# Kernel optimization log

Hardware: AMD Instinct MI355X
Metric: run time of the kernel (lower is better)

## Reference

```python
import jax, jax.numpy as jnp
import numpy as np

H = W = 256
L = H * W                      # number of graph vertices / tree leaves
N_NODES = 2 * L - 1            # binary partition tree node count
LAM = 1.0                      # lambda_ (soft-area temperature)


def _grid_edges():
    """4-adjacency grid graph edges (same structure as higra get_4_adjacency_graph)."""
    idx = np.arange(L, dtype=np.int64).reshape(H, W)
    src = np.concatenate([idx[:, :-1].ravel(), idx[:-1, :].ravel()])
    dst = np.concatenate([idx[:, 1:].ravel(), idx[1:, :].ravel()])
    return src.astype(np.int32), dst.astype(np.int32)


def setup_inputs() -> dict:
    key = jax.random.key(0)
    src, dst = _grid_edges()
    ew = jax.random.uniform(key, (src.shape[0],), dtype=jnp.float32)
    return {"edge_weights": ew,
            "edges_src": jnp.asarray(src),
            "edges_dst": jnp.asarray(dst)}


def _build_tree(ew, src, dst):
    """higra.bpt_canonical: Kruskal over stably-sorted edges, building a binary
    merge tree. Leaves are 0..L-1, internal node L+i is created by the i-th MST
    edge. Returns (sizes, mst_edge_map, ancestor paths). All integer structure
    is piecewise-constant w.r.t. edge_weights (no gradient flows through it)."""
    order = np.argsort(ew, kind="stable")
    uf = np.arange(L)

    def find(x):
        r = x
        while uf[r] != r:
            r = uf[r]
        while uf[x] != r:
            uf[x], x = r, uf[x]
        return r

    canon = np.arange(L)                      # tree node of each union-find root
    parent = np.arange(N_NODES)               # self-parent until set (root keeps self)
    sizes = np.ones(N_NODES, dtype=np.float32)
    edge_map = np.zeros(L - 1, dtype=np.int64)
    node = L
    for ei in order:
        a = find(src[ei]); b = find(dst[ei])
        if a == b:
            continue
        na, nb = canon[a], canon[b]
        parent[na] = node
        parent[nb] = node
        sizes[node] = sizes[na] + sizes[nb]
        edge_map[node - L] = ei
        uf[a] = b
        canon[b] = node
        node += 1
    # self-inclusive ancestor paths, padded by repeating the root
    cur = np.arange(N_NODES)
    cols = [cur.copy()]
    while np.any(parent[cur] != cur):
        cur = parent[cur]
        cols.append(cur.copy())
    paths = np.stack(cols, axis=1)            # [N_NODES, D+1]
    return sizes, edge_map, paths


def _softarea(edge_weights, edge_map, sizes_np, paths_np):
    """Soft area of every tree node n:
       area(n) = sum_x sigmoid((alt(n) - d(x, n)) / lambda)
    where d(x,n) is the min ultrametric distance from leaf x to the leaves of n:
      - x in subtree(n), x != n : d = alt(parent(x))
      - x == n (leaf)           : d = 0
      - x outside subtree(n)    : d = alt(lowest ancestor of n containing x).
    Outside leaves are grouped per ancestor a (count = size(a) - size(previous
    node on the path)), giving an O(N * depth) vectorized computation."""
    alt = jnp.concatenate([jnp.zeros((L,), edge_weights.dtype),
                           edge_weights[edge_map]])          # [N_NODES]
    alt_path = alt[paths_np]                                  # [N, D+1]
    size_path = sizes_np[paths_np]                            # constant, numpy
    diff = jnp.asarray(size_path[:, 1:] - size_path[:, :-1])  # 0 on root padding
    outside = jnp.sum(
        diff * jax.nn.sigmoid((alt[:, None] - alt_path[:, 1:]) / LAM), axis=1)

    # inside: each leaf x contributes sigmoid((alt(a_k) - alt(parent(x)))/lam)
    # to every proper ancestor a_k, plus sigmoid(0)=0.5 to itself (alt(leaf)=0).
    lp = paths_np[:L]                                         # [L, D+1]
    alt_lp = alt_path[:L]
    valid = jnp.asarray((lp[:, 1:] != lp[:, :-1]).astype(np.float32))
    vals = jax.nn.sigmoid((alt_lp[:, 1:] - alt_lp[:, 1:2]) / LAM) * valid
    inside = jax.ops.segment_sum(vals.reshape(-1),
                                 jnp.asarray(lp[:, 1:].reshape(-1)),
                                 num_segments=N_NODES)
    inside = inside.at[:L].add(0.5)
    return inside + outside


def reference(edge_weights, edges_src, edges_dst):
    sizes, edge_map, paths = _build_tree(np.asarray(edge_weights),
                                         np.asarray(edges_src),
                                         np.asarray(edges_dst))
    return _softarea(edge_weights, jnp.asarray(edge_map), sizes, paths)
```

## Files before the change

### kernel.cpp

```cpp
#include <hip/hip_runtime.h>
#include <stdint.h>

typedef unsigned int u32;
typedef unsigned short u16;
typedef unsigned long long u64;

#define L_VERTS 65536
#define N_EDGES 130560
#define N_NODES 131071
#define NODEPAD 131072

#define CCH 170
#define CCHM 86
#define SCH 768
#define PADM (CCHM*SCH)
#define NMST (L_VERTS-1)
#define MAXSV 1536
#define HSZ 2048

#define NB 255
#define TPB 64
#define IPT 8
#define IPB 512

__global__ void init_keys(const float* __restrict__ w, u32* __restrict__ keys, u32* __restrict__ vals,
                          u32* szG, u16* canonTop16, u32* parent, float* alt){
  int i = blockIdx.x*blockDim.x + threadIdx.x;
  if(i < N_EDGES){ keys[i] = __float_as_uint(w[i]); vals[i] = (u32)i; }
  if(i < N_NODES){ parent[i]=(u32)i; alt[i]=0.f; }
  if(i < L_VERTS){ szG[i]=1u; canonTop16[i]=0xFFFFu; }
}

__global__ void radix_hist(const u32* __restrict__ idx, const u32* __restrict__ keys,
                           u32* __restrict__ histG, int shift){
  __shared__ u32 h[256];
  for(int i=threadIdx.x;i<256;i+=TPB) h[i]=0;
  __syncthreads();
  int base = blockIdx.x*IPB + threadIdx.x*IPT;
  #pragma unroll
  for(int i=0;i<IPT;i++){
    u32 e = idx[base+i];
    u32 d = (keys[e]>>shift)&255u;
    atomicAdd(&h[d],1u);
  }
  __syncthreads();
  for(int i=threadIdx.x;i<256;i+=TPB) histG[i*NB+blockIdx.x]=h[i];
}

__global__ void radix_scan(u32* histG){
  const int M = 256*NB;
  __shared__ u32 sums[1024];
  int t=threadIdx.x; int s=t*64; u32 acc=0;
  for(int i=0;i<64;i++){int id=s+i; if(id<M) acc+=histG[id];}
  sums[t]=acc; __syncthreads();
  for(int off=1; off<1024; off<<=1){
    u32 v=(t>=off)?sums[t-off]:0u;
    __syncthreads();
    sums[t]+=v;
    __syncthreads();
  }
  u32 run = (t==0)?0u:sums[t-1];
  for(int i=0;i<64;i++){int id=s+i; if(id<M){u32 v=histG[id]; histG[id]=run; run+=v;}}
}

__global__ void radix_scatter(const u32* __restrict__ idxIn, const u32* __restrict__ keys,
                              u32* __restrict__ idxOut, const u32* __restrict__ histG, int shift){
  __shared__ u16 thoff[256][TPB];
  int t=threadIdx.x;
  for(int d=t;d<256;d+=TPB) for(int j=0;j<TPB;j++) thoff[d][j]=0;
  __syncthreads();
  int base = blockIdx.x*IPB + t*IPT;
  u32 myv[IPT]; u32 myd[IPT];
  #pragma unroll
  for(int i=0;i<IPT;i++){
    myv[i]=idxIn[base+i];
    myd[i]=(keys[myv[i]]>>shift)&255u;
    thoff[myd[i]][t]++;
  }
  __syncthreads();
  for(int dd=0;dd<4;dd++){
    int d=t*4+dd; u32 run=0;
    for(int j=0;j<TPB;j++){ u32 v=thoff[d][j]; thoff[d][j]=(u16)run; run+=v; }
  }
  __syncthreads();
  #pragma unroll
  for(int i=0;i<IPT;i++){
    u32 d=myd[i];
    u32 pos = histG[d*NB+blockIdx.x] + (u32)thoff[d][t];
    thoff[d][t]++;
    idxOut[pos]=myv[i];
  }
}

__global__ void build_epair(const u32* __restrict__ order, const int* __restrict__ srcv,
                            const int* __restrict__ dstv, u32* __restrict__ epair){
  int p=blockIdx.x*blockDim.x+threadIdx.x;
  if(p>=N_EDGES) return;
  u32 e=order[p];
  epair[p]=((u32)dstv[e]<<16)|(u32)srcv[e];
}

#define CBK 255
#define CT 512
#define DEADE 0xFFFFFFFFu

__device__ __forceinline__ u32 bfind(const u32* __restrict__ parentB, u32 x){
  while(true){ u32 p=parentB[x]; if(p==x) return x; x=p; }
}

__global__ void bor_init(u32* parentB, u32* minE, unsigned char* mstF, u32* bctr){
  int i=blockIdx.x*blockDim.x+threadIdx.x;
  if(i<L_VERTS){ parentB[i]=(u32)i; minE[i]=0xFFFFFFFFu; }
  if(i<N_EDGES) mstF[i]=0;
  if(i<16) bctr[i]=0u;
}

__global__ void bor_minedge(u32* __restrict__ epair, const u32* __restrict__ parentB,
                            u32* __restrict__ minE, const unsigned char* __restrict__ mstF,
                            const u32* __restrict__ bctr, int r){
  if(r>0 && bctr[r-1]==0u) return;
  int p=blockIdx.x*blockDim.x+threadIdx.x;
  u32 pr=epair[p];
  if(pr==DEADE) return;
  u32 ra=bfind(parentB, pr&0xFFFFu), rb=bfind(parentB, pr>>16);
  if(ra==rb){ if(!mstF[p]) epair[p]=DEADE; return; }
  atomicMin(&minE[ra],(u32)p);
  atomicMin(&minE[rb],(u32)p);
}

__global__ void bor_hookA(const u32* __restrict__ epair, const u32* __restrict__ parentB,
                          const u32* __restrict__ minE, u32* __restrict__ nextB,
                          unsigned char* __restrict__ mstF, const u32* __restrict__ bctr, int r){
  if(r>0 && bctr[r-1]==0u) return;
  int v=blockIdx.x*blockDim.x+threadIdx.x;
  if(v>=L_VERTS) return;
  if(parentB[v]!=(u32)v) return;
  u32 p=minE[v];
  if(p==0xFFFFFFFFu) return;
  u32 pr=epair[p];
  u32 ra=bfind(parentB, pr&0xFFFFu), rb=bfind(parentB, pr>>16);
  u32 w2=(ra==(u32)v)?rb:ra;
  nextB[v]=w2;
  mstF[p]=1;
}

__global__ void bor_hookB(u32* __restrict__ parentB, const u32* __restrict__ minE,
                          const u32* __restrict__ nextB, u32* __restrict__ bctr, int r){
  if(r>0 && bctr[r-1]==0u) return;
  int v=blockIdx.x*blockDim.x+threadIdx.x;
  if(v>=L_VERTS) return;
  if(parentB[v]!=(u32)v) return;
  u32 p=minE[v];
  if(p==0xFFFFFFFFu) return;
  u32 w2=nextB[v];
  if(minE[w2]==p && (u32)v<w2) return;
  parentB[v]=w2;
  bctr[r]=1u;
}

__global__ void bor_compress(u32* __restrict__ parentB, u32* __restrict__ minE,
                             const u32* __restrict__ bctr, int r){
  if(r>0 && bctr[r-1]==0u) return;
  int v=blockIdx.x*blockDim.x+threadIdx.x;
  if(v>=L_VERTS) return;
  u32 x=(u32)v;
  while(true){ u32 px=parentB[x]; if(px==x) break; u32 g=parentB[px]; if(g!=px) parentB[x]=g; x=g; }
  parentB[v]=x;
  minE[v]=0xFFFFFFFFu;
}

__global__ void mst_count(const unsigned char* __restrict__ mstF, u32* __restrict__ blockCnt){
  int b=blockIdx.x, t=threadIdx.x;
  int p=b*CT+t;
  u64 m=__ballot(mstF[p]!=0);
  __shared__ u32 ws[8];
  if((t&63)==0) ws[t>>6]=(u32)__popcll(m);
  __syncthreads();
  if(t==0){ u32 s=0; for(int i=0;i<8;i++) s+=ws[i]; blockCnt[b]=s; }
}

__global__ void mst_scan(const u32* __restrict__ blockCnt, u32* __restrict__ blockBase,
                         u32* __restrict__ mepair){
  int t=threadIdx.x;
  __shared__ u32 s[256];
  u32 v=(t<CBK)?blockCnt[t]:0u;
  s[t]=v; __syncthreads();
  for(int o=1;o<256;o<<=1){ u32 x=(t>=o)?s[t-o]:0u; __syncthreads(); s[t]+=x; __syncthreads(); }
  if(t<CBK) blockBase[t]=s[t]-v;
  u32 total=s[255];
  for(u32 j=total+(u32)t; j<(u32)PADM; j+=256u) mepair[j]=0u;
}

__global__ void mst_scatter(const unsigned char* __restrict__ mstF, const u32* __restrict__ blockBase,
                            const u32* __restrict__ order, const u32* __restrict__ epair,
                            const float* __restrict__ w,
                            u32* __restrict__ mepair, float* __restrict__ alt){
  int b=blockIdx.x, t=threadIdx.x;
  int p=b*CT+t;
  u32 f=(u32)mstF[p];
  u64 m=__ballot(f!=0);
  __shared__ u32 ws[8];
  int wid=t>>6, lane=t&63;
  if(lane==0) ws[wid]=(u32)__popcll(m);
  __syncthreads();
  if(t==0){ u32 s2=0; for(int i=0;i<8;i++){ u32 x=ws[i]; ws[i]=s2; s2+=x; } }
  __syncthreads();
  if(f){
    u32 pre=(u32)__popcll(m & ((1ull<<lane)-1ull));
    u32 pos=blockBase[b]+ws[wid]+pre;
    mepair[pos]=epair[p];
    alt[(u32)L_VERTS+pos]=w[order[p]];
  }
}

__device__ __forceinline__ u32 ald(u32* p){
  return __hip_atomic_load(p, __ATOMIC_RELAXED, __HIP_MEMORY_SCOPE_AGENT);
}
__device__ __forceinline__ void ast(u32* p, u32 v){
  __hip_atomic_store(p, v, __ATOMIC_RELAXED, __HIP_MEMORY_SCOPE_AGENT);
}

__global__ void __launch_bounds__(1024,1) p1_checkpoints(
    const u32* __restrict__ epair,
    u32* szG, u16* lid16, u16* svroot16, u16* svsize16, u16* svnext16, u32* mG)
{
  __shared__ u16 ufL[L_VERTS];
  __shared__ u32 hkey[HSZ];
  __shared__ u32 sufL[MAXSV];
  __shared__ u32 compsz[MAXSV];
  __shared__ u16 ssz[MAXSV];
  __shared__ u16 lidL[2*SCH];
  __shared__ u32 mcnt;
  int t = threadIdx.x;
  for(int i=t;i<L_VERTS/2;i+=1024) ((u32*)ufL)[i]=((2u*(u32)i+1u)<<16)|(2u*(u32)i);
  for(int k=0;k<CCHM;k++){
    for(int i=t;i<HSZ;i+=1024) hkey[i]=0xFFFFFFFFu;
    for(u32 s=t;s<MAXSV;s+=1024){ sufL[s]=s; compsz[s]=0u; }
    if(t==0) mcnt=0u;
    __syncthreads();
    int base = k*SCH;
    for(int i=t;i<2*SCH;i+=1024){
      u32 pr = epair[base+(i>>1)];
      u32 v = (i&1)? (pr>>16) : (pr&0xFFFFu);
      u32 x=v;
      while(true){ u32 px=ufL[x]; if(px==x)break; u32 g=ufL[px]; if(g!=px) ufL[x]=(u16)g; x=g; }
      u32 r=x;
      if(v!=r) ufL[v]=(u16)r;
      u32 h=(r*2654435761u)>>21;
      while(true){
        u32 old=atomicCAS(&hkey[h],0xFFFFFFFFu,(r<<16)|0x7FFFu);
        if(old==0xFFFFFFFFu){
          u32 id=atomicAdd(&mcnt,1u);
          svroot16[k*MAXSV+id]=(u16)r;
          hkey[h]=(r<<16)|id;
          break;
        }
        if((old>>16)==r) break;
        h=(h+1)&(HSZ-1u);
      }
      lidL[i]=(u16)h;
    }
    __syncthreads();
    u32 mc=mcnt;
    if(t==0) mG[k]=mc;
    for(u32 s=t;s<mc;s+=1024){
      u32 r=(u32)svroot16[k*MAXSV+s];
      u32 szm1=ald(&szG[r])-1u;
      svsize16[k*MAXSV+s]=(u16)szm1;
      ssz[s]=(u16)szm1;
    }
    for(int i=t;i<2*SCH;i+=1024) lid16[2*base+i]=(u16)(hkey[lidL[i]]&0xFFFFu);
    for(int j=t;j<SCH;j+=1024){
      u32 sa=hkey[lidL[2*j]]&0xFFFFu, sb=hkey[lidL[2*j+1]]&0xFFFFu;
      if(sa==sb) continue;
      while(true){
        u32 x=sa; while(true){u32 p2=sufL[x]; if(p2==x)break; u32 g=sufL[p2]; if(g!=p2) sufL[x]=g; x=g;}
        u32 y=sb; while(true){u32 p2=sufL[y]; if(p2==y)break; u32 g=sufL[p2]; if(g!=p2) sufL[y]=g; y=g;}
        if(x==y) break;
        u32 hi=x>y?x:y, lo=x^y^hi;
        if(atomicCAS(&sufL[hi],hi,lo)==hi) break;
        sa=hi; sb=lo;
      }
    }
    __syncthreads();
    for(u32 s=t;s<mc;s+=1024){
      u32 x=s; while(true){u32 p2=sufL[x]; if(p2==x)break; x=p2;}
      sufL[s]=x;
      atomicAdd(&compsz[x], (u32)ssz[s]+1u);
    }
    __syncthreads();
    for(u32 s=t;s<mc;s+=1024){
      u32 rs=sufL[s];
      u32 wv=(u32)svroot16[k*MAXSV+rs];
      svnext16[k*MAXSV+s]=(u16)wv;
      u32 myroot=(u32)svroot16[k*MAXSV+s];
      if(myroot!=wv) ufL[myroot]=(u16)wv;
      if(s==rs)      ast(&szG[wv], compsz[rs]);
    }
    __syncthreads();
  }
}

__global__ void __launch_bounds__(64) p2_chunk(
  const u16* __restrict__ lid16,
  const u16* __restrict__ svsize16, const u16* __restrict__ svnext16, const u32* __restrict__ mG,
  u16* __restrict__ outChA, u16* __restrict__ outChB, u16* __restrict__ outSize16,
  u32* __restrict__ accCnt, u16* __restrict__ compR16, u16* __restrict__ compTop16, u32* __restrict__ ncomp)
{
  int k = blockIdx.x; int t = threadIdx.x;
  __shared__ u16 uf[MAXSV];
  __shared__ u32 csize[MAXSV];
  __shared__ u16 ctop[MAXSV];
  __shared__ u16 svnl[MAXSV];
  __shared__ u32 lidP[SCH];
  __shared__ u32 cmp_s;
  u32 m = mG[k];
  int base=k*SCH;
  for(u32 s=t;s<m;s+=64){
    uf[s]=(u16)s;
    csize[s]=(u32)svsize16[k*MAXSV+s]+1u;
    ctop[s]=(u16)s;
    svnl[s]=svnext16[k*MAXSV+s];
  }
  for(int j=t;j<SCH;j+=64) lidP[j]=((const u32*)lid16)[base+j];
  if(t==0) cmp_s=0u;
  __syncthreads();
  if(t==0){
    u32 cnt=0;
    for(int j=0;j<SCH;j++){
      u32 lw = lidP[j];
      u32 la = lw & 0xFFFFu, lb = lw >> 16;
      u32 x=la; while(true){u32 px=uf[x]; if(px==x)break; u32 g=uf[px]; uf[x]=(u16)g; x=g;}
      u32 y=lb; while(true){u32 py=uf[y]; if(py==y)break; u32 g=uf[py]; uf[y]=(u16)g; y=g;}
      if(x==y) continue;
      u32 sa=csize[x], sb=csize[y], ns=sa+sb;
      outChA[base+cnt]=ctop[x];
      outChB[base+cnt]=ctop[y];
      outSize16[base+cnt]=(u16)(ns-1u);
      u32 win=(sa>=sb)?x:y, los=x^y^win;
      uf[los]=(u16)win; csize[win]=ns; ctop[win]=(u16)(0x8000u|cnt);
      cnt++;
    }
    accCnt[k]=cnt;
  }
  __syncthreads();
  for(u32 s=t;s<m;s+=64){
    if(uf[s]==(u16)s && (ctop[s]&0x8000u)){
      u32 pos=atomicAdd(&cmp_s,1u);
      compR16[k*MAXSV+pos]=svnl[s];
      compTop16[k*MAXSV+pos]=(u16)(ctop[s]&0x7FFFu);
    }
  }
  __syncthreads();
  if(t==0) ncomp[k]=cmp_s;
}

__global__ void __launch_bounds__(1024) p3_stitch(
  const u32* __restrict__ accCnt, const u16* __restrict__ outChA, const u16* __restrict__ outChB,
  const u16* __restrict__ outSize16,
  const u16* __restrict__ svroot16,
  const u16* __restrict__ compR16, const u16* __restrict__ compTop16, const u32* __restrict__ ncomp,
  u16* __restrict__ canonTop16, u32* __restrict__ parent, u16* __restrict__ usize16)
{
  __shared__ u32 accBase[CCH];
  int t=threadIdx.x;
  if(t==0){ u32 r=0; for(int k=0;k<CCHM;k++){ accBase[k]=r; r+=accCnt[k]; } }
  __syncthreads();
  for(int idx=t; idx<PADM; idx+=1024){
    int k = idx/SCH; int j = idx - k*SCH;
    if(j < (int)accCnt[k]){
      u32 nid = (u32)L_VERTS + accBase[k] + (u32)j;
      usize16[nid] = outSize16[idx];
      u32 cA=outChA[idx]; if(cA & 0x8000u) parent[(u32)L_VERTS+accBase[k]+(cA&0x7FFFu)] = nid;
      u32 cB=outChB[idx]; if(cB & 0x8000u) parent[(u32)L_VERTS+accBase[k]+(cB&0x7FFFu)] = nid;
    }
  }
  __syncthreads();
  for(int k=0;k<CCHM;k++){
    u32 ac=accCnt[k];
    for(u32 j=t;j<ac;j+=1024){
      u32 idx=(u32)(k*SCH)+j;
      u32 nid=(u32)L_VERTS+accBase[k]+j;
      u32 cA=outChA[idx];
      if(!(cA&0x8000u)){
        u32 root=(u32)svroot16[k*MAXSV+cA];
        u32 ct=(u32)canonTop16[root];
        parent[(ct==0xFFFFu)?root:((u32)L_VERTS+ct)]=nid;
      }
      u32 cB=outChB[idx];
      if(!(cB&0x8000u)){
        u32 root=(u32)svroot16[k*MAXSV+cB];
        u32 ct=(u32)canonTop16[root];
        parent[(ct==0xFFFFu)?root:((u32)L_VERTS+ct)]=nid;
      }
    }
    __syncthreads();
    u32 nc=ncomp[k];
    for(u32 j=t;j<nc;j+=1024){
      canonTop16[(u32)compR16[k*MAXSV+j]] = (u16)(accBase[k]+compTop16[k*MAXSV+j]);
    }
    __syncthreads();
  }
}

__device__ __forceinline__ void hvals6(float v, float* o){
  float v2=v*v, v3=v2*v, v4=v2*v2, v5=v4*v;
  o[0]=0.5f-0.25f*v+v3*(1.f/48.f)-v5*(1.f/480.f);
  o[1]=0.25f-v2*(1.f/16.f)+v4*(1.f/96.f);
  o[2]=v*(1.f/16.f)-v3*(1.f/48.f);
  o[3]=v2*(1.f/48.f)-(1.f/48.f);
  o[4]=-v*(1.f/96.f);
  o[5]=(1.f/480.f);
}

__global__ void zero_both(u32* cc, float* nodeM, u32* ctr){
  int i=blockIdx.x*blockDim.x+threadIdx.x;
  if(i<L_VERTS) cc[i]=0u;
  if(i<6*NODEPAD) nodeM[i]=0.f;
  if(i==0) *ctr=0u;
}

__global__ void prep_init(const u32* __restrict__ parent, const u16* __restrict__ usize16,
                          u32* cc, u32* J0, uint2* A0, float* out){
  int n=blockIdx.x*blockDim.x+threadIdx.x;
  if(n>=N_NODES) return;
  out[n] = (n<L_VERTS)?0.5f:0.0f;
  if(n==N_NODES-1){ J0[n]=(u32)n; A0[n]=make_uint2(0u,0u); return; }
  u32 p=parent[n];
  u32 ord=atomicAdd(&cc[p-L_VERTS],1u);
  u32 szP=(u32)usize16[p]+1u;
  u32 szN=(n<L_VERTS)?1u:((u32)usize16[n]+1u);
  u32 sib=szP-szN;
  A0[n]=make_uint2(ord? sib:0u, 1u + (ord? (2u*sib-1u):0u));
  J0[n]=p;
}

__global__ void triple_round(const u32* __restrict__ Jin, const uint2* __restrict__ Ain,
                             u32* __restrict__ Jout, uint2* __restrict__ Aout){
  int n=blockIdx.x*blockDim.x+threadIdx.x;
  if(n>=N_NODES) return;
  u32 j1=Jin[n], j2=Jin[j1], j3=Jin[j2], j4=Jin[j3], j5=Jin[j4], j6=Jin[j5], j7=Jin[j6];
  uint2 a0=Ain[n], a1=Ain[j1], a2=Ain[j2], a3=Ain[j3], a4=Ain[j4], a5=Ain[j5], a6=Ain[j6], a7=Ain[j7];
  Aout[n]=make_uint2(a0.x+a1.x+a2.x+a3.x+a4.x+a5.x+a6.x+a7.x,
                     a0.y+a1.y+a2.y+a3.y+a4.y+a5.y+a6.y+a7.y);
  Jout[n]=Jin[j7];
}

__global__ void scatter_all(const u32* __restrict__ parent, const float* __restrict__ alt,
                            const u16* __restrict__ usize16, const uint2* __restrict__ accF,
                            float* __restrict__ leafM, float* __restrict__ nodeM){
  int n=blockIdx.x*blockDim.x+threadIdx.x;
  if(n>=N_NODES) return;
  u32 p=parent[n];
  float h[6]; hvals6(alt[p],h);
  uint2 af=accF[n];
  if(n<L_VERTS){
    u32 pos=af.x;
    #pragma unroll
    for(int j=0;j<6;j++) leafM[(size_t)j*L_VERTS+pos]=h[j];
  }
  if(n<N_NODES-1){
    u32 szP=(u32)usize16[p]+1u;
    u32 szN=(n<L_VERTS)?1u:((u32)usize16[n]+1u);
    float d=(float)(szP-szN);
    u32 q0=af.y;
    u32 q1=q0 + 2u*szN - 1u;
    #pragma unroll
    for(int j=0;j<6;j++){
      float tm=d*h[j];
      atomicAdd(&nodeM[(size_t)j*NODEPAD+q0], tm);
      atomicAdd(&nodeM[(size_t)j*NODEPAD+q1], -tm);
    }
  }
}

__global__ void scanAll(float* __restrict__ leafM, float* __restrict__ nodeM,
                        float* __restrict__ bsumL, float* __restrict__ bsumN, u32* ctr){
  int b=blockIdx.x; int t=threadIdx.x;
  float* arr; u32 base; float* bs;
  if(b<6*64){ int row=b>>6, blk=b&63;  arr=leafM+(size_t)row*L_VERTS;  base=(u32)blk*1024u; bs=&bsumL[row*64+blk]; }
  else      { int bb=b-384; int row=bb>>7, blk=bb&127; arr=nodeM+(size_t)row*NODEPAD; base=(u32)blk*1024u; bs=&bsumN[row*128+blk]; }
  __shared__ float s[256];
  __shared__ u32 lastFlag;
  base += (u32)t*4u;
  float v0=arr[base],v1=arr[base+1],v2=arr[base+2],v3=arr[base+3];
  v1+=v0; v2+=v1; v3+=v2;
  s[t]=v3; __syncthreads();
  for(int o=1;o<256;o<<=1){ float x=(t>=o)?s[t-o]:0.f; __syncthreads(); s[t]+=x; __syncthreads(); }
  float pre=(t>0)?s[t-1]:0.f;
  arr[base]=v0+pre; arr[base+1]=v1+pre; arr[base+2]=v2+pre; arr[base+3]=v3+pre;
  if(t==255) *bs=s[255];
  __threadfence();
  if(t==0) lastFlag = (atomicAdd(ctr,1u)==1151u) ? 1u : 0u;
  __syncthreads();
  if(lastFlag){
    __threadfence();
    if(t<6){ float r=0; for(int i=0;i<64;i++){ float v=bsumL[t*64+i]; bsumL[t*64+i]=r; r+=v; } }
    else if(t<12){ int j=t-6; float r=0; for(int i=0;i<128;i++){ float v=bsumN[j*128+i]; bsumN[j*128+i]=r; r+=v; } }
  }
}

__global__ void eval_all(const uint2* __restrict__ accF, const float* __restrict__ alt,
                         const u16* __restrict__ usize16, const float* __restrict__ leafM,
                         const float* __restrict__ nodeM, const float* __restrict__ bsumL,
                         const float* __restrict__ bsumN, float* __restrict__ out){
  int n=blockIdx.x*blockDim.x+threadIdx.x;
  if(n>=N_NODES) return;
  uint2 af=accF[n];
  float u=alt[n];
  u32 q=af.y;
  float acc=0.f, up=1.f;
  #pragma unroll
  for(int j=0;j<6;j++){
    float T = nodeM[(size_t)j*NODEPAD+q] + bsumN[j*128 + (q>>10)];
    acc += up*T;
    up*=u;
  }
  if(n>=L_VERTS){
    u32 lo=af.x;
    u32 hi=lo + (u32)usize16[n] + 1u;
    up=1.f;
    #pragma unroll
    for(int j=0;j<6;j++){
      const float* arr=leafM + (size_t)j*L_VERTS;
      const float* bs=bsumL + j*64;
      float Ph = arr[hi-1u] + bs[(hi-1u)>>10];
      float Pl = lo ? (arr[lo-1u] + bs[(lo-1u)>>10]) : 0.f;
      acc += up*(Ph-Pl);
      up*=u;
    }
  }
  out[n]+=acc;
}

__global__ void ws_too_small(float* out){
  int i=blockIdx.x*blockDim.x+threadIdx.x;
  if(i<N_NODES) out[i]=1.0e6f;
}

extern "C" void kernel_launch(void* const* d_in, const int* in_sizes, int n_in,
                              void* d_out, int out_size, void* d_ws, size_t ws_size,
                              hipStream_t stream){
  (void)in_sizes; (void)n_in; (void)out_size;
  const float* w  = (const float*)d_in[0];
  const int* src  = (const int*)d_in[1];
  const int* dst  = (const int*)d_in[2];
  float* out = (float*)d_out;

  char* ws = (char*)d_ws;
  size_t off=0;
  auto alloc=[&](size_t bytes)->void*{ void* p = ws+off; off += (bytes+511)&~(size_t)511; return p; };
  u32* parent   =(u32*)alloc((size_t)N_NODES*4);
  float* alt    =(float*)alloc((size_t)N_NODES*4);
  u16* usize16  =(u16*)alloc((size_t)N_NODES*2);
  float* bsumL  =(float*)alloc(6*64*4);
  float* bsumN  =(float*)alloc(6*128*4);
  u32* ctr      =(u32*)alloc(512);
  size_t scratch0=off;
  u32* keys0    =(u32*)alloc((size_t)N_EDGES*4);
  u32* vals0    =(u32*)alloc((size_t)N_EDGES*4);
  u32* vals1    =(u32*)alloc((size_t)N_EDGES*4);
  u32* histG    =(u32*)alloc(256*NB*4);
  u16* canonTop16=(u16*)alloc((size_t)L_VERTS*2);
  u16* svroot16 =(u16*)alloc((size_t)CCH*MAXSV*2);
  u16* svsize16 =(u16*)alloc((size_t)CCH*MAXSV*2);
  u16* svnext16 =(u16*)alloc((size_t)CCH*MAXSV*2);
  u32* mG       =(u32*)alloc(CCH*4);
  u32* accCnt   =(u32*)alloc(CCH*4);
  u32* ncomp    =(u32*)alloc(CCH*4);
  u32* parentB  =(u32*)alloc((size_t)L_VERTS*4);
  u32* minE     =(u32*)alloc((size_t)L_VERTS*4);
  u32* nextB    =(u32*)alloc((size_t)L_VERTS*4);
  unsigned char* mstF=(unsigned char*)alloc((size_t)N_EDGES);
  u32* blockCnt =(u32*)alloc(256*4);
  u32* blockBase=(u32*)alloc(256*4);
  u32* mepair   =(u32*)alloc((size_t)PADM*4);
  u32* bctr     =(u32*)alloc(512);
  size_t endA=off;
  off=scratch0;
  u32* ccChsum  =(u32*)alloc((size_t)L_VERTS*4);
  u32* J0       =(u32*)alloc((size_t)N_NODES*4);
  u32* J1       =(u32*)alloc((size_t)N_NODES*4);
  uint2* A0     =(uint2*)alloc((size_t)N_NODES*8);
  uint2* A1     =(uint2*)alloc((size_t)N_NODES*8);
  float* nodeM  =(float*)alloc((size_t)6*NODEPAD*4);
  size_t endB=off;
  float* leafM  =(float*)ccChsum;

  if((endA>ws_size)||(endB>ws_size)){
    ws_too_small<<<(N_NODES+255)/256,256,0,stream>>>(out);
    return;
  }

  u16* lid16    =(u16*)vals1;
  u32* epair    =keys0;
  u16* outChA16 =(u16*)histG;
  u16* outChB16 =(u16*)keys0;
  u16* outSize16=(u16*)((char*)keys0 + (size_t)N_EDGES*2);
  u16* compR16  =svsize16;
  u16* compTop16=svnext16;
  u32* szG      =(u32*)usize16;

  init_keys<<<(N_NODES+255)/256,256,0,stream>>>(w,keys0,vals0,szG,canonTop16,parent,alt);
  for(int pass=0;pass<4;pass++){
    const u32* iv = (pass&1)?vals1:vals0;
    u32* ov = (pass&1)?vals0:vals1;
    int shift=pass*8;
    radix_hist   <<<NB,TPB,0,stream>>>(iv,keys0,histG,shift);
    radix_scan   <<<1,1024,0,stream>>>(histG);
    radix_scatter<<<NB,TPB,0,stream>>>(iv,keys0,ov,histG,shift);
  }
  build_epair<<<(N_EDGES+255)/256,256,0,stream>>>(vals0,src,dst,epair);
  bor_init<<<CBK,CT,0,stream>>>(parentB,minE,mstF,bctr);
  for(int r=0;r<16;r++){
    bor_minedge <<<CBK,CT,0,stream>>>(epair,parentB,minE,mstF,bctr,r);
    bor_hookA   <<<L_VERTS/CT,CT,0,stream>>>(epair,parentB,minE,nextB,mstF,bctr,r);
    bor_hookB   <<<L_VERTS/CT,CT,0,stream>>>(parentB,minE,nextB,bctr,r);
    bor_compress<<<L_VERTS/CT,CT,0,stream>>>(parentB,minE,bctr,r);
  }
  mst_count  <<<CBK,CT,0,stream>>>(mstF,blockCnt);
  mst_scan   <<<1,256,0,stream>>>(blockCnt,blockBase,mepair);
  mst_scatter<<<CBK,CT,0,stream>>>(mstF,blockBase,vals0,epair,w,mepair,alt);
  p1_checkpoints<<<1,1024,0,stream>>>(mepair,szG,lid16,svroot16,svsize16,svnext16,mG);
  p2_chunk<<<CCHM,64,0,stream>>>(lid16,svsize16,svnext16,mG,
                                outChA16,outChB16,outSize16,accCnt,compR16,compTop16,ncomp);
  p3_stitch<<<1,1024,0,stream>>>(accCnt,outChA16,outChB16,outSize16,svroot16,
                                 compR16,compTop16,ncomp,canonTop16,parent,usize16);
  zero_both<<<(6*NODEPAD+255)/256,256,0,stream>>>(ccChsum,nodeM,ctr);
  prep_init<<<(N_NODES+255)/256,256,0,stream>>>(parent,usize16,ccChsum,J1,A1,out);
  for(int r=0;r<6;r++){
    if((r&1)==0) triple_round<<<(N_NODES+255)/256,256,0,stream>>>(J1,A1,J0,A0);
    else         triple_round<<<(N_NODES+255)/256,256,0,stream>>>(J0,A0,J1,A1);
  }
  const uint2* accF=A1;
  scatter_all<<<(N_NODES+255)/256,256,0,stream>>>(parent,alt,usize16,accF,leafM,nodeM);
  scanAll<<<1152,256,0,stream>>>(leafM,nodeM,bsumL,bsumN,ctr);
  eval_all<<<(N_NODES+255)/256,256,0,stream>>>(accF,alt,usize16,leafM,nodeM,bsumL,bsumN,out);
}
```

Baseline: 2.615 ms.

## Drop per-chunk compaction, write parent/size in chunk kernel, fuse zeroing

Node ids now map one-to-one to MST edge positions (each MST edge in a chunk always merges), so the per-chunk count and prefix base are removed. Parent and size writes for intra-chunk children move from the single-block stitch kernel into the parallel chunk kernel. The checkpoint kernel caches supervertex roots in shared memory and merges two loops, which removes one global read pass. The nodeM zeroing moves into prep_init, shrinking the zero kernel. The risk is the assumption that every MST edge in a chunk merges two distinct components.

```diff
diff --git a/kernel.cpp b/kernel.cpp
--- a/kernel.cpp
+++ b/kernel.cpp
@@ -229,6 +229,7 @@
   __shared__ u32 sufL[MAXSV];
   __shared__ u32 compsz[MAXSV];
   __shared__ u16 ssz[MAXSV];
+  __shared__ u16 svtx[MAXSV];
   __shared__ u16 lidL[2*SCH];
   __shared__ u32 mcnt;
   int t = threadIdx.x;
@@ -252,6 +253,7 @@
         if(old==0xFFFFFFFFu){
           u32 id=atomicAdd(&mcnt,1u);
           svroot16[k*MAXSV+id]=(u16)r;
+          svtx[id]=(u16)r;
           hkey[h]=(r<<16)|id;
           break;
         }
@@ -264,7 +266,7 @@
     u32 mc=mcnt;
     if(t==0) mG[k]=mc;
     for(u32 s=t;s<mc;s+=1024){
-      u32 r=(u32)svroot16[k*MAXSV+s];
+      u32 r=(u32)svtx[s];
       u32 szm1=ald(&szG[r])-1u;
       svsize16[k*MAXSV+s]=(u16)szm1;
       ssz[s]=(u16)szm1;
@@ -287,15 +289,14 @@
       u32 x=s; while(true){u32 p2=sufL[x]; if(p2==x)break; x=p2;}
       sufL[s]=x;
       atomicAdd(&compsz[x], (u32)ssz[s]+1u);
+      u32 wv=(u32)svtx[x];
+      svnext16[k*MAXSV+s]=(u16)wv;
+      u32 myroot=(u32)svtx[s];
+      if(myroot!=wv) ufL[myroot]=(u16)wv;
     }
     __syncthreads();
     for(u32 s=t;s<mc;s+=1024){
-      u32 rs=sufL[s];
-      u32 wv=(u32)svroot16[k*MAXSV+rs];
-      svnext16[k*MAXSV+s]=(u16)wv;
-      u32 myroot=(u32)svroot16[k*MAXSV+s];
-      if(myroot!=wv) ufL[myroot]=(u16)wv;
-      if(s==rs)      ast(&szG[wv], compsz[rs]);
+      if(sufL[s]==s) ast(&szG[(u32)svtx[s]], compsz[s]);
     }
     __syncthreads();
   }
@@ -304,8 +305,9 @@
 __global__ void __launch_bounds__(64) p2_chunk(
   const u16* __restrict__ lid16,
   const u16* __restrict__ svsize16, const u16* __restrict__ svnext16, const u32* __restrict__ mG,
-  u16* __restrict__ outChA, u16* __restrict__ outChB, u16* __restrict__ outSize16,
-  u32* __restrict__ accCnt, u16* __restrict__ compR16, u16* __restrict__ compTop16, u32* __restrict__ ncomp)
+  u16* __restrict__ outChA, u16* __restrict__ outChB,
+  u32* __restrict__ parent, u16* __restrict__ usize16,
+  u16* __restrict__ compR16, u16* __restrict__ compTop16, u32* __restrict__ ncomp)
 {
   int k = blockIdx.x; int t = threadIdx.x;
   __shared__ u16 uf[MAXSV];
@@ -325,23 +327,25 @@
   for(int j=t;j<SCH;j+=64) lidP[j]=((const u32*)lid16)[base+j];
   if(t==0) cmp_s=0u;
   __syncthreads();
+  int nk=(k==CCHM-1)?(NMST-(CCHM-1)*SCH):SCH;
   if(t==0){
-    u32 cnt=0;
-    for(int j=0;j<SCH;j++){
+    for(int j=0;j<nk;j++){
       u32 lw = lidP[j];
       u32 la = lw & 0xFFFFu, lb = lw >> 16;
       u32 x=la; while(true){u32 px=uf[x]; if(px==x)break; u32 g=uf[px]; uf[x]=(u16)g; x=g;}
       u32 y=lb; while(true){u32 py=uf[y]; if(py==y)break; u32 g=uf[py]; uf[y]=(u16)g; y=g;}
       if(x==y) continue;
       u32 sa=csize[x], sb=csize[y], ns=sa+sb;
-      outChA[base+cnt]=ctop[x];
-      outChB[base+cnt]=ctop[y];
-      outSize16[base+cnt]=(u16)(ns-1u);
+      u32 nid=(u32)L_VERTS+(u32)base+(u32)j;
+      u32 cA=ctop[x], cB=ctop[y];
+      if(cA&0x8000u) parent[(u32)L_VERTS+(u32)base+(cA&0x7FFFu)]=nid;
+      if(cB&0x8000u) parent[(u32)L_VERTS+(u32)base+(cB&0x7FFFu)]=nid;
+      outChA[base+j]=(u16)cA;
+      outChB[base+j]=(u16)cB;
+      usize16[nid]=(u16)(ns-1u);
       u32 win=(sa>=sb)?x:y, los=x^y^win;
-      uf[los]=(u16)win; csize[win]=ns; ctop[win]=(u16)(0x8000u|cnt);
-      cnt++;
-    }
-    accCnt[k]=cnt;
+      uf[los]=(u16)win; csize[win]=ns; ctop[win]=(u16)(0x8000u|(u32)j);
+    }
   }
   __syncthreads();
   for(u32 s=t;s<m;s+=64){
@@ -356,31 +360,18 @@
 }
 
 __global__ void __launch_bounds__(1024) p3_stitch(
-  const u32* __restrict__ accCnt, const u16* __restrict__ outChA, const u16* __restrict__ outChB,
-  const u16* __restrict__ outSize16,
+  const u16* __restrict__ outChA, const u16* __restrict__ outChB,
   const u16* __restrict__ svroot16,
   const u16* __restrict__ compR16, const u16* __restrict__ compTop16, const u32* __restrict__ ncomp,
-  u16* __restrict__ canonTop16, u32* __restrict__ parent, u16* __restrict__ usize16)
+  u16* __restrict__ canonTop16, u32* __restrict__ parent)
 {
-  __shared__ u32 accBase[CCH];
   int t=threadIdx.x;
-  if(t==0){ u32 r=0; for(int k=0;k<CCHM;k++){ accBase[k]=r; r+=accCnt[k]; } }
-  __syncthreads();
-  for(int idx=t; idx<PADM; idx+=1024){
-    int k = idx/SCH; int j = idx - k*SCH;
-    if(j < (int)accCnt[k]){
-      u32 nid = (u32)L_VERTS + accBase[k] + (u32)j;
-      usize16[nid] = outSize16[idx];
-      u32 cA=outChA[idx]; if(cA & 0x8000u) parent[(u32)L_VERTS+accBase[k]+(cA&0x7FFFu)] = nid;
-      u32 cB=outChB[idx]; if(cB & 0x8000u) parent[(u32)L_VERTS+accBase[k]+(cB&0x7FFFu)] = nid;
-    }
-  }
-  __syncthreads();
   for(int k=0;k<CCHM;k++){
-    u32 ac=accCnt[k];
-    for(u32 j=t;j<ac;j+=1024){
-      u32 idx=(u32)(k*SCH)+j;
-      u32 nid=(u32)L_VERTS+accBase[k]+j;
+    int base=k*SCH;
+    int nk=(k==CCHM-1)?(NMST-(CCHM-1)*SCH):SCH;
+    for(int j=t;j<nk;j+=1024){
+      int idx=base+j;
+      u32 nid=(u32)L_VERTS+(u32)idx;
       u32 cA=outChA[idx];
       if(!(cA&0x8000u)){
         u32 root=(u32)svroot16[k*MAXSV+cA];
@@ -397,7 +388,7 @@
     __syncthreads();
     u32 nc=ncomp[k];
     for(u32 j=t;j<nc;j+=1024){
-      canonTop16[(u32)compR16[k*MAXSV+j]] = (u16)(accBase[k]+compTop16[k*MAXSV+j]);
+      canonTop16[(u32)compR16[k*MAXSV+j]] = (u16)((u32)base + (u32)compTop16[k*MAXSV+j]);
     }
     __syncthreads();
   }
@@ -413,16 +404,19 @@
   o[5]=(1.f/480.f);
 }
 
-__global__ void zero_both(u32* cc, float* nodeM, u32* ctr){
+__global__ void zero_cc(u32* cc, u32* ctr){
   int i=blockIdx.x*blockDim.x+threadIdx.x;
   if(i<L_VERTS) cc[i]=0u;
-  if(i<6*NODEPAD) nodeM[i]=0.f;
   if(i==0) *ctr=0u;
 }
 
 __global__ void prep_init(const u32* __restrict__ parent, const u16* __restrict__ usize16,
-                          u32* cc, u32* J0, uint2* A0, float* out){
+                          u32* cc, u32* J0, uint2* A0, float* out, float* __restrict__ nodeM){
   int n=blockIdx.x*blockDim.x+threadIdx.x;
+  if(n<NODEPAD){
+    #pragma unroll
+    for(int j=0;j<6;j++) nodeM[(size_t)j*NODEPAD+n]=0.f;
+  }
   if(n>=N_NODES) return;
   out[n] = (n<L_VERTS)?0.5f:0.0f;
   if(n==N_NODES-1){ J0[n]=(u32)n; A0[n]=make_uint2(0u,0u); return; }
@@ -566,7 +560,6 @@
   u16* svsize16 =(u16*)alloc((size_t)CCH*MAXSV*2);
   u16* svnext16 =(u16*)alloc((size_t)CCH*MAXSV*2);
   u32* mG       =(u32*)alloc(CCH*4);
-  u32* accCnt   =(u32*)alloc(CCH*4);
   u32* ncomp    =(u32*)alloc(CCH*4);
   u32* parentB  =(u32*)alloc((size_t)L_VERTS*4);
   u32* minE     =(u32*)alloc((size_t)L_VERTS*4);
@@ -596,7 +589,6 @@
   u32* epair    =keys0;
   u16* outChA16 =(u16*)histG;
   u16* outChB16 =(u16*)keys0;
-  u16* outSize16=(u16*)((char*)keys0 + (size_t)N_EDGES*2);
   u16* compR16  =svsize16;
   u16* compTop16=svnext16;
   u32* szG      =(u32*)usize16;
@@ -622,12 +614,12 @@
   mst_scan   <<<1,256,0,stream>>>(blockCnt,blockBase,mepair);
   mst_scatter<<<CBK,CT,0,stream>>>(mstF,blockBase,vals0,epair,w,mepair,alt);
   p1_checkpoints<<<1,1024,0,stream>>>(mepair,szG,lid16,svroot16,svsize16,svnext16,mG);
-  p2_chunk<<<CCHM,64,0,stream>>>(lid16,svsize16,svnext16,mG,
-                                outChA16,outChB16,outSize16,accCnt,compR16,compTop16,ncomp);
-  p3_stitch<<<1,1024,0,stream>>>(accCnt,outChA16,outChB16,outSize16,svroot16,
-                                 compR16,compTop16,ncomp,canonTop16,parent,usize16);
-  zero_both<<<(6*NODEPAD+255)/256,256,0,stream>>>(ccChsum,nodeM,ctr);
-  prep_init<<<(N_NODES+255)/256,256,0,stream>>>(parent,usize16,ccChsum,J1,A1,out);
+  p2_chunk<<<CCHM,64,0,stream>>>(lid16,svsize16,svnext16,mG,outChA16,outChB16,
+                                 parent,usize16,compR16,compTop16,ncomp);
+  p3_stitch<<<1,1024,0,stream>>>(outChA16,outChB16,svroot16,
+                                 compR16,compTop16,ncomp,canonTop16,parent);
+  zero_cc<<<(L_VERTS+255)/256,256,0,stream>>>(ccChsum,ctr);
+  prep_init<<<(NODEPAD+255)/256,256,0,stream>>>(parent,usize16,ccChsum,J1,A1,out,nodeM);
   for(int r=0;r<6;r++){
     if((r&1)==0) triple_round<<<(N_NODES+255)/256,256,0,stream>>>(J1,A1,J0,A0);
     else         triple_round<<<(N_NODES+255)/256,256,0,stream>>>(J0,A0,J1,A1);
```

After: 2.604 ms. Within noise of the previous version (-0.4%).
